# Kernel optimization log

Hardware: AMD Instinct MI355X
Metric: run time of the kernel (lower is better)

The kernel has to match this reference:

```python
import jax, jax.numpy as jnp
import numpy as np

LN_EPS = 1e-5   # torch LayerNorm default
NRM_EPS = 1e-8  # normalizer-state epsilon in mLSTMCell


def setup_inputs() -> dict:
    key = jax.random.key(0)
    ks = jax.random.split(key, 3)
    B, T, H, L, O = 32, 256, 1024, 4, 256
    x = jax.random.normal(ks[0], (B, T, H), dtype=jnp.float32)
    # 6 projections per layer in order (q, k, v, i, f, o); Linear stored as [in, out]
    W = jax.random.normal(ks[1], (L, 6, H, H), dtype=jnp.float32) * 0.02
    b = jnp.zeros((L, 6, H), dtype=jnp.float32)
    ln_g = jnp.ones((L, 6, H), dtype=jnp.float32)
    ln_b = jnp.zeros((L, 6, H), dtype=jnp.float32)
    fc_w = jax.random.normal(ks[2], (H, O), dtype=jnp.float32) * 0.02
    fc_b = jnp.zeros((O,), dtype=jnp.float32)
    return {"x": x, "W": W, "b": b, "ln_g": ln_g, "ln_b": ln_b,
            "fc_w": fc_w, "fc_b": fc_b}


def _layer_norm(z, g, beta):
    # z: [6, B, H]; g, beta: [6, H]
    mu = z.mean(-1, keepdims=True)
    var = z.var(-1, keepdims=True)
    return (z - mu) * jax.lax.rsqrt(var + LN_EPS) * g[:, None, :] + beta[:, None, :]


def _cell(x_in, h_prev, c_prev, n_prev, Wl, bl, gl, betal):
    # x_in: [B, H]; states: [B, H]; Wl: [6, H, H]
    z = jnp.einsum('bh,jhd->jbd', x_in, Wl) + bl[:, None, :]
    z = _layer_norm(z, gl, betal)
    q, k, v, zi, zf, zo = z  # q is computed by the original cell but unused
    i = jnp.exp(zi)
    f = jax.nn.sigmoid(zf)
    o = jax.nn.sigmoid(zo)
    # kv_interaction = outer(k, v); sum over dim=1 == sum(k) * v (same math, no [B,H,H])
    kv_sum = k.sum(-1, keepdims=True) * v
    c = f * c_prev + i * kv_sum
    n = f * n_prev + i * k
    n_hat = n / (jnp.linalg.norm(n, axis=-1, keepdims=True) + NRM_EPS)
    h = o * jnp.tanh(c * n_hat)
    return h, c, n


def _mlstm_forward(x, W, b, ln_g, ln_b, fc_w, fc_b):
    B, T, H = x.shape
    L = W.shape[0]
    h0 = jnp.zeros((L, B, H), x.dtype)
    init = (h0, h0, h0)  # (h, c, n)

    def step(carry, x_t):
        h, c, n = carry
        layer_in = x_t
        hs, cs, ns = [], [], []
        for l in range(L):  # small fixed layer count
            h_l, c_l, n_l = _cell(layer_in, h[l], c[l], n[l],
                                  W[l], b[l], ln_g[l], ln_b[l])
            if l > 0:  # residual connection (use_residual=True)
                h_l = h_l + layer_in
            layer_in = h_l
            hs.append(h_l); cs.append(c_l); ns.append(n_l)
        return (jnp.stack(hs), jnp.stack(cs), jnp.stack(ns)), None

    (h, c, n), _ = jax.lax.scan(step, init, jnp.swapaxes(x, 0, 1))
    # output[-1] == top-layer hidden at the final timestep
    out = h[-1] @ fc_w + fc_b  # [B, O]
    return out, (h, c, n)


def reference(x, W, b, ln_g, ln_b, fc_w, fc_b):
    return _mlstm_forward(x, W, b, ln_g, ln_b, fc_w, fc_b)
```

## Files before the change

### kernel.cpp

```cpp
#include <hip/hip_runtime.h>
#include <hip/hip_bf16.h>
#include <math.h>

#define H 1024
#define B 32
#define T 256
#define L 4
#define O 256
#define SEGLEN 16
#define NSEG (T / SEGLEN)

typedef _Float16 half8 __attribute__((ext_vector_type(8)));
typedef _Float16 half4 __attribute__((ext_vector_type(4)));
typedef float f32x4 __attribute__((ext_vector_type(4)));

#define X_PK_OFF   0
#define HB0_OFF    8388608
#define HB1_OFF    16777216
#define WT2_OFF    25165824
#define Z16_OFF    46137344
#define SEGA_OFF   88080384
#define SEGBC_OFF  89128960
#define SEGBN_OFF  90177536
#define STATS_OFF  91226112
#define CARC_OFF   91422720
#define CARN_OFF   92471296
#define FCP_OFF    93519872

__global__ __launch_bounds__(256) void pack_w(const float* __restrict__ W,
                                              _Float16* __restrict__ Wt2) {
  int tile = blockIdx.x;
  int m_idx = tile >> 8;
  int kt = (tile >> 4) & 15, ntt = tile & 15;
  int l = m_idx / 5, jj = m_idx % 5;
  const float* Wf = W + ((size_t)(l * 6 + jj + 1) << 20);
  _Float16* out = Wt2 + ((size_t)m_idx << 20);
  __shared__ float ts[64][65];
  int k0 = kt * 64, n0 = ntt * 64;
#pragma unroll
  for (int s = 0; s < 16; ++s) {
    int e = threadIdx.x + s * 256;
    int kk = e >> 6, col = e & 63;
    ts[kk][col] = Wf[(size_t)(k0 + kk) * H + n0 + col];
  }
  __syncthreads();
#pragma unroll
  for (int gi = 0; gi < 2; ++gi) {
    int g = threadIdx.x * 2 + gi;
    int l64 = g & 63, ksl = (g >> 6) & 1, ntl = g >> 7;
    int nn = l64 & 15, kh = l64 >> 4;
    half8 tmp;
#pragma unroll
    for (int e = 0; e < 8; ++e)
      tmp[e] = (_Float16)ts[ksl * 32 + kh * 8 + e][ntl * 16 + nn];
    *(half8*)&out[(size_t)((ntt * 4 + ntl) * 32 + kt * 2 + ksl) * 512 + (size_t)l64 * 8] = tmp;
  }
}

__global__ __launch_bounds__(256) void pack_x(const float* __restrict__ x,
                                              _Float16* __restrict__ x_pk) {
  int t = blockIdx.x;
  __shared__ float ld[32][257];
  for (int c = 0; c < 4; ++c) {
#pragma unroll
    for (int s = 0; s < 32; ++s) {
      int e2 = threadIdx.x + s * 256;
      int b = e2 >> 8, col = e2 & 255;
      ld[b][col] = x[((size_t)b * T + t) * H + c * 256 + col];
    }
    __syncthreads();
#pragma unroll
    for (int s3 = 0; s3 < 4; ++s3) {
      int gg = threadIdx.x * 4 + s3;
      int l64 = gg & 63, ksl = (gg >> 6) & 7, bt = gg >> 9;
      int nn = l64 & 15, kh = l64 >> 4;
      int b = bt * 16 + nn;
      half8 tmp;
#pragma unroll
      for (int e = 0; e < 8; ++e)
        tmp[e] = (_Float16)ld[b][ksl * 32 + kh * 8 + e];
      *(half8*)&x_pk[(size_t)t * 32768 + (size_t)bt * 16384 +
                     (size_t)(c * 8 + ksl) * 512 + (size_t)l64 * 8] = tmp;
    }
    __syncthreads();
  }
}

__global__ __launch_bounds__(512) void gemm_big(
    const _Float16* __restrict__ A_pk, const _Float16* __restrict__ Wl,
    _Float16* __restrict__ z16) {
  int raw = blockIdx.x;
  int xcd = raw & 7, c = raw >> 3;
  int bm = (xcd >> 1) * 16 + (c & 15);
  int bn = (xcd & 1) * 10 + (c >> 4);
  int w = threadIdx.x >> 6, lane = threadIdx.x & 63;
  int wm = w >> 2, wn = w & 3;

  __shared__ _Float16 smem[24576];

  int j = bn >> 2;
  const _Float16* gsrc[3];
  int ldst[3];
#pragma unroll
  for (int q = 0; q < 3; ++q) {
    int f = w * 3 + q;
    if (f < 8) {
      gsrc[q] = A_pk + (size_t)(bm * 8 + f) * 16384 + lane * 8;
      ldst[q] = f * 512 + lane * 8;
    } else {
      int nf = f - 8;
      gsrc[q] = Wl + ((size_t)j << 20) + (size_t)((bn & 3) * 16 + nf) * 16384 + lane * 8;
      ldst[q] = 4096 + nf * 512 + lane * 8;
    }
  }

  half8 stA[3], stB[3];
#pragma unroll
  for (int q = 0; q < 3; ++q) stA[q] = *(const half8*)(gsrc[q]);
#pragma unroll
  for (int q = 0; q < 3; ++q) *(half8*)&smem[ldst[q]] = stA[q];
#pragma unroll
  for (int q = 0; q < 3; ++q) stA[q] = *(const half8*)(gsrc[q] + 512);
  __syncthreads();

  f32x4 acc[4][4] = {};
  int ardo = wm * 2048 + lane * 8;
  int brdo = 4096 + wn * 2048 + lane * 8;

  for (int ks = 0; ks < 32; ks += 2) {
    {
      if (ks + 2 < 32) {
#pragma unroll
        for (int q = 0; q < 3; ++q)
          stB[q] = *(const half8*)(gsrc[q] + (size_t)(ks + 2) * 512);
      }
      half8 a[4], b[4];
#pragma unroll
      for (int i = 0; i < 4; ++i) a[i] = *(const half8*)&smem[ardo + i * 512];
#pragma unroll
      for (int i = 0; i < 4; ++i) b[i] = *(const half8*)&smem[brdo + i * 512];
#pragma unroll
      for (int i = 0; i < 4; ++i)
#pragma unroll
        for (int jf = 0; jf < 4; ++jf)
          acc[i][jf] = __builtin_amdgcn_mfma_f32_16x16x32_f16(a[i], b[jf], acc[i][jf], 0, 0, 0);
#pragma unroll
      for (int q = 0; q < 3; ++q) *(half8*)&smem[12288 + ldst[q]] = stA[q];
      asm volatile("s_waitcnt lgkmcnt(0)" ::: "memory");
      __builtin_amdgcn_s_barrier();
      __builtin_amdgcn_sched_barrier(0);
    }
    {
      if (ks + 3 < 32) {
#pragma unroll
        for (int q = 0; q < 3; ++q)
          stA[q] = *(const half8*)(gsrc[q] + (size_t)(ks + 3) * 512);
      }
      half8 a[4], b[4];
#pragma unroll
      for (int i = 0; i < 4; ++i) a[i] = *(const half8*)&smem[12288 + ardo + i * 512];
#pragma unroll
      for (int i = 0; i < 4; ++i) b[i] = *(const half8*)&smem[12288 + brdo + i * 512];
#pragma unroll
      for (int i = 0; i < 4; ++i)
#pragma unroll
        for (int jf = 0; jf < 4; ++jf)
          acc[i][jf] = __builtin_amdgcn_mfma_f32_16x16x32_f16(a[i], b[jf], acc[i][jf], 0, 0, 0);
      if (ks + 2 < 32) {
#pragma unroll
        for (int q = 0; q < 3; ++q) *(half8*)&smem[ldst[q]] = stB[q];
        asm volatile("s_waitcnt lgkmcnt(0)" ::: "memory");
        __builtin_amdgcn_s_barrier();
        __builtin_amdgcn_sched_barrier(0);
      }
    }
  }
  __syncthreads();

  _Float16 (*cz)[264] = (_Float16(*)[264])smem;
  int hb0 = (bn & 3) * 256;
  for (int p = 0; p < 2; ++p) {
    if (p) __syncthreads();
    if (wm == p) {
#pragma unroll
      for (int i = 0; i < 4; ++i)
#pragma unroll
        for (int jf = 0; jf < 4; ++jf)
#pragma unroll
          for (int r = 0; r < 4; ++r)
            cz[i * 16 + (lane >> 4) * 4 + r][wn * 64 + jf * 16 + (lane & 15)] =
                (_Float16)acc[i][jf][r];
    }
    __syncthreads();
#pragma unroll
    for (int s = 0; s < 4; ++s) {
      int e = threadIdx.x + s * 512;
      int r = e >> 5, h8 = e & 31;
      int m_local = bm * 128 + p * 64 + r;
      half8 vv = *(const half8*)&cz[r][h8 * 8];
      *(half8*)&z16[((size_t)m_local * 5 + j) * 1024 + hb0 + h8 * 8] = vv;
    }
  }
}

__global__ __launch_bounds__(256) void scan_p1fused(
    const _Float16* __restrict__ z16, const float* __restrict__ bias,
    const float* __restrict__ ln_g, const float* __restrict__ ln_b,
    float* __restrict__ stats, float* __restrict__ segA,
    float* __restrict__ segBc, float* __restrict__ segBn, int l) {
  int seg = blockIdx.x >> 5, b = blockIdx.x & 31;
  int tid = threadIdx.x, h0 = tid * 4;

  float bz[5][4], gg[5][4], bb[5][4];
#pragma unroll
  for (int jj = 0; jj < 5; ++jj) {
    float4 t1 = *(const float4*)&bias[(size_t)(l * 6 + 1 + jj) * H + h0];
    float4 t2 = *(const float4*)&ln_g[(size_t)(l * 6 + 1 + jj) * H + h0];
    float4 t3 = *(const float4*)&ln_b[(size_t)(l * 6 + 1 + jj) * H + h0];
    bz[jj][0] = t1.x; bz[jj][1] = t1.y; bz[jj][2] = t1.z; bz[jj][3] = t1.w;
    gg[jj][0] = t2.x; gg[jj][1] = t2.y; gg[jj][2] = t2.z; gg[jj][3] = t2.w;
    bb[jj][0] = t3.x; bb[jj][1] = t3.y; bb[jj][2] = t3.z; bb[jj][3] = t3.w;
  }

  float A[4] = {1.f, 1.f, 1.f, 1.f};
  float bc[4] = {0.f, 0.f, 0.f, 0.f};
  float bn[4] = {0.f, 0.f, 0.f, 0.f};
  __shared__ float sb[4][13];

  half4 zr[5];
  {
    int row0 = (seg * SEGLEN) * 32 + b;
#pragma unroll
    for (int jj = 0; jj < 5; ++jj)
      zr[jj] = *(const half4*)&z16[((size_t)row0 * 5 + jj) * 1024 + h0];
  }

  for (int u = 0; u < SEGLEN; ++u) {
    int row = (seg * SEGLEN + u) * 32 + b;
    half4 zc[5];
#pragma unroll
    for (int jj = 0; jj < 5; ++jj) zc[jj] = zr[jj];
    if (u + 1 < SEGLEN) {
      int rown = (seg * SEGLEN + u + 1) * 32 + b;
#pragma unroll
      for (int jj = 0; jj < 5; ++jj)
        zr[jj] = *(const half4*)&z16[((size_t)rown * 5 + jj) * 1024 + h0];
    }
    float v[5][4];
    float red[13];
#pragma unroll
    for (int jj = 0; jj < 5; ++jj) {
      float s = 0.f, sq = 0.f;
#pragma unroll
      for (int e = 0; e < 4; ++e) {
        float val = (float)zc[jj][e] + bz[jj][e];
        v[jj][e] = val;
        s += val;
        sq += val * val;
      }
      red[jj * 2] = s;
      red[jj * 2 + 1] = sq;
      if (jj == 0) {
        red[10] = v[0][0] * gg[0][0] + v[0][1] * gg[0][1] +
                  v[0][2] * gg[0][2] + v[0][3] * gg[0][3];
        red[11] = gg[0][0] + gg[0][1] + gg[0][2] + gg[0][3];
        red[12] = bb[0][0] + bb[0][1] + bb[0][2] + bb[0][3];
      }
    }
#pragma unroll
    for (int off = 32; off; off >>= 1)
#pragma unroll
      for (int q = 0; q < 13; ++q) red[q] += __shfl_xor(red[q], off);
    if ((tid & 63) == 0) {
#pragma unroll
      for (int q = 0; q < 13; ++q) sb[tid >> 6][q] = red[q];
    }
    __syncthreads();
    float st[13];
#pragma unroll
    for (int q = 0; q < 13; ++q)
      st[q] = sb[0][q] + sb[1][q] + sb[2][q] + sb[3][q];
    __syncthreads();

    float mus[5], rss[5];
#pragma unroll
    for (int jj = 0; jj < 5; ++jj) {
      float mu = st[jj * 2] * (1.0f / H);
      float var = st[jj * 2 + 1] * (1.0f / H) - mu * mu;
      mus[jj] = mu;
      rss[jj] = rsqrtf(var + 1e-5f);
    }
    float ksum = rss[0] * (st[10] - mus[0] * st[11]) + st[12];
    if (tid < 12) {
      float val;
      if (tid < 10) val = (tid & 1) ? rss[tid >> 1] : mus[tid >> 1];
      else if (tid == 10) val = ksum;
      else val = 0.f;
      stats[(size_t)row * 12 + tid] = val;
    }
#pragma unroll
    for (int e = 0; e < 4; ++e) {
      float k   = (v[0][e] - mus[0]) * rss[0] * gg[0][e] + bb[0][e];
      float vv  = (v[1][e] - mus[1]) * rss[1] * gg[1][e] + bb[1][e];
      float zi_ = (v[2][e] - mus[2]) * rss[2] * gg[2][e] + bb[2][e];
      float zf_ = (v[3][e] - mus[3]) * rss[3] * gg[3][e] + bb[3][e];
      float iv = __expf(zi_);
      float fv = 1.f / (1.f + __expf(-zf_));
      A[e] *= fv;
      bn[e] = fv * bn[e] + iv * k;
      bc[e] = fv * bc[e] + iv * (ksum * vv);
    }
  }
  size_t so = ((size_t)seg * 32 + b) * 1024 + h0;
  *(float4*)&segA[so]  = make_float4(A[0], A[1], A[2], A[3]);
  *(float4*)&segBn[so] = make_float4(bn[0], bn[1], bn[2], bn[3]);
  *(float4*)&segBc[so] = make_float4(bc[0], bc[1], bc[2], bc[3]);
}

__global__ __launch_bounds__(256) void scan_p2(
    const float* __restrict__ segA, const float* __restrict__ segBc,
    const float* __restrict__ segBn, float* __restrict__ carC,
    float* __restrict__ carN) {
  int idx = blockIdx.x * 256 + threadIdx.x;
  int h = idx & 1023, b = idx >> 10;
  float cc = 0.f, nn = 0.f;
#pragma unroll
  for (int seg = 0; seg < NSEG; ++seg) {
    size_t coff = (size_t)seg * 32768 + (size_t)b * 1024 + h;
    carC[coff] = cc;
    carN[coff] = nn;
    size_t so = ((size_t)seg * 32 + b) * 1024 + h;
    float a = segA[so];
    cc = segBc[so] + a * cc;
    nn = segBn[so] + a * nn;
  }
}

__global__ __launch_bounds__(256) void final_scan(
    const _Float16* __restrict__ z16, const float* __restrict__ stats,
    const float* __restrict__ bias, const float* __restrict__ ln_g,
    const float* __restrict__ ln_b, const float* __restrict__ carC,
    const float* __restrict__ carN, const _Float16* __restrict__ hin,
    _Float16* __restrict__ hout, float* __restrict__ out, int l) {
  int seg = blockIdx.x >> 5, b = blockIdx.x & 31;
  int tid = threadIdx.x, h0 = tid * 4;

  float bz[5][4], gg[5][4], bb[5][4];
#pragma unroll
  for (int jj = 0; jj < 5; ++jj) {
    float4 t1 = *(const float4*)&bias[(size_t)(l * 6 + 1 + jj) * H + h0];
    float4 t2 = *(const float4*)&ln_g[(size_t)(l * 6 + 1 + jj) * H + h0];
    float4 t3 = *(const float4*)&ln_b[(size_t)(l * 6 + 1 + jj) * H + h0];
    bz[jj][0] = t1.x; bz[jj][1] = t1.y; bz[jj][2] = t1.z; bz[jj][3] = t1.w;
    gg[jj][0] = t2.x; gg[jj][1] = t2.y; gg[jj][2] = t2.z; gg[jj][3] = t2.w;
    bb[jj][0] = t3.x; bb[jj][1] = t3.y; bb[jj][2] = t3.z; bb[jj][3] = t3.w;
  }

  size_t coff = (size_t)seg * 32768 + (size_t)b * 1024 + h0;
  float4 cC4 = *(const float4*)&carC[coff];
  float4 cN4 = *(const float4*)&carN[coff];
  float c_[4] = {cC4.x, cC4.y, cC4.z, cC4.w};
  float n_[4] = {cN4.x, cN4.y, cN4.z, cN4.w};

  size_t hfoff = (size_t)(b >> 4) * 16384 + (size_t)(h0 >> 5) * 512 +
                 (size_t)((((h0 & 31) >> 3) * 16) + (b & 15)) * 8 + (h0 & 7);
  __shared__ float sbuf[2][4];

  half4 zr[5];
  {
    int row0 = (seg * SEGLEN) * 32 + b;
#pragma unroll
    for (int jj = 0; jj < 5; ++jj)
      zr[jj] = *(const half4*)&z16[((size_t)row0 * 5 + jj) * 1024 + h0];
  }

  for (int u = 0; u < SEGLEN; ++u) {
    int t = seg * SEGLEN + u;
    int row = t * 32 + b;
    half4 zc[5];
#pragma unroll
    for (int jj = 0; jj < 5; ++jj) zc[jj] = zr[jj];
    if (u + 1 < SEGLEN) {
      int rown = (t + 1) * 32 + b;
#pragma unroll
      for (int jj = 0; jj < 5; ++jj)
        zr[jj] = *(const half4*)&z16[((size_t)rown * 5 + jj) * 1024 + h0];
    }
    half4 rin;
    if (l > 0) rin = *(const half4*)&hin[(size_t)t * 32768 + hfoff];

    const float* st = stats + (size_t)row * 12;
    float mu0 = st[0], rs0 = st[1], mu1 = st[2], rs1 = st[3];
    float mu2 = st[4], rs2 = st[5], mu3 = st[6], rs3 = st[7];
    float mu4 = st[8], rs4 = st[9], ksum = st[10];

    float ss = 0.f;
#pragma unroll
    for (int e = 0; e < 4; ++e) {
      float k   = ((float)zc[0][e] + bz[0][e] - mu0) * rs0 * gg[0][e] + bb[0][e];
      float v   = ((float)zc[1][e] + bz[1][e] - mu1) * rs1 * gg[1][e] + bb[1][e];
      float zi_ = ((float)zc[2][e] + bz[2][e] - mu2) * rs2 * gg[2][e] + bb[2][e];
      float zf_ = ((float)zc[3][e] + bz[3][e] - mu3) * rs3 * gg[3][e] + bb[3][e];
      float iv = __expf(zi_);
      float fv = 1.f / (1.f + __expf(-zf_));
      n_[e] = fv * n_[e] + iv * k;
      c_[e] = fv * c_[e] + iv * (ksum * v);
      ss += n_[e] * n_[e];
    }
#pragma unroll
    for (int off = 32; off; off >>= 1) ss += __shfl_down(ss, off);
    if ((tid & 63) == 0) sbuf[u & 1][tid >> 6] = ss;
    __syncthreads();
    float nrm = sbuf[u & 1][0] + sbuf[u & 1][1] + sbuf[u & 1][2] + sbuf[u & 1][3];
    float rn = 1.f / (sqrtf(nrm) + 1e-8f);

    float hh[4];
#pragma unroll
    for (int e = 0; e < 4; ++e) {
      float zo_ = ((float)zc[4][e] + bz[4][e] - mu4) * rs4 * gg[4][e] + bb[4][e];
      float ov = 1.f / (1.f + __expf(-zo_));
      float targ = c_[e] * (n_[e] * rn);
      float e2 = __expf(-2.f * fabsf(targ));
      float th = copysignf((1.f - e2) / (1.f + e2), targ);
      hh[e] = ov * th + ((l > 0) ? (float)rin[e] : 0.f);
    }
    half4 hx;
    hx[0] = (_Float16)hh[0]; hx[1] = (_Float16)hh[1];
    hx[2] = (_Float16)hh[2]; hx[3] = (_Float16)hh[3];
    *(half4*)&hout[(size_t)t * 32768 + hfoff] = hx;

    if (t == T - 1) {
      *(float4*)&out[8192 + (size_t)l * 32768 + (size_t)b * 1024 + h0] =
          make_float4(hh[0], hh[1], hh[2], hh[3]);
      *(float4*)&out[8192 + 131072 + ((size_t)(l * B) + b) * 1024 + h0] =
          make_float4(c_[0], c_[1], c_[2], c_[3]);
      *(float4*)&out[8192 + 262144 + ((size_t)(l * B) + b) * 1024 + h0] =
          make_float4(n_[0], n_[1], n_[2], n_[3]);
    }
  }
}

__global__ __launch_bounds__(256) void fc_part(
    const float* __restrict__ out_h, const float* __restrict__ fc_w,
    float* __restrict__ partial) {
  int b = blockIdx.x >> 3, kh = blockIdx.x & 7;
  int o = threadIdx.x;
  const float* hr = out_h + (size_t)b * 1024 + kh * 128;
  const float* wp = fc_w + (size_t)kh * 128 * O + o;
  float acc = 0.f;
#pragma unroll 8
  for (int h = 0; h < 128; ++h)
    acc = fmaf(hr[h], wp[(size_t)h * O], acc);
  partial[((size_t)kh * 32 + b) * O + o] = acc;
}

__global__ __launch_bounds__(256) void fc_reduce(
    const float* __restrict__ partial, const float* __restrict__ fc_b,
    float* __restrict__ out) {
  int b = blockIdx.x, o = threadIdx.x;
  float acc = fc_b[o];
#pragma unroll
  for (int kh = 0; kh < 8; ++kh)
    acc += partial[((size_t)kh * 32 + b) * O + o];
  out[(size_t)b * O + o] = acc;
}

extern "C" void kernel_launch(void* const* d_in, const int* in_sizes, int n_in,
                              void* d_out, int out_size, void* d_ws, size_t ws_size,
                              hipStream_t stream) {
  const float* x    = (const float*)d_in[0];
  const float* W    = (const float*)d_in[1];
  const float* bias = (const float*)d_in[2];
  const float* ln_g = (const float*)d_in[3];
  const float* ln_b = (const float*)d_in[4];
  const float* fc_w = (const float*)d_in[5];
  const float* fc_b = (const float*)d_in[6];
  float* out = (float*)d_out;
  _Float16* wsh = (_Float16*)d_ws;

  _Float16* x_pk = wsh + X_PK_OFF;
  _Float16* hb[2] = {wsh + HB0_OFF, wsh + HB1_OFF};
  _Float16* Wt2  = wsh + WT2_OFF;
  _Float16* z16  = wsh + Z16_OFF;
  float* segA  = (float*)(wsh + SEGA_OFF);
  float* segBc = (float*)(wsh + SEGBC_OFF);
  float* segBn = (float*)(wsh + SEGBN_OFF);
  float* stats = (float*)(wsh + STATS_OFF);
  float* carC  = (float*)(wsh + CARC_OFF);
  float* carN  = (float*)(wsh + CARN_OFF);
  float* fcp   = (float*)(wsh + FCP_OFF);

  pack_w<<<5120, 256, 0, stream>>>(W, Wt2);
  pack_x<<<256, 256, 0, stream>>>(x, x_pk);

  for (int l = 0; l < L; ++l) {
    const _Float16* A_in = (l == 0) ? x_pk : hb[(l - 1) & 1];
    _Float16* h_out = hb[l & 1];
    const _Float16* Wl = Wt2 + ((size_t)(l * 5) << 20);
    gemm_big<<<1280, 512, 0, stream>>>(A_in, Wl, z16);
    scan_p1fused<<<512, 256, 0, stream>>>(z16, bias, ln_g, ln_b, stats,
                                          segA, segBc, segBn, l);
    scan_p2<<<128, 256, 0, stream>>>(segA, segBc, segBn, carC, carN);
    final_scan<<<512, 256, 0, stream>>>(z16, stats, bias, ln_g, ln_b,
                                        carC, carN, A_in, h_out, out, l);
  }
  fc_part<<<256, 256, 0, stream>>>(out + 8192 + 3 * 32768, fc_w, fcp);
  fc_reduce<<<B, 256, 0, stream>>>(fcp, fc_b, out);
}
```

Before: 767.1 us.

## Halve scan segment length, merge pack kernels, slim per-step reductions

Scan segments shrink from 16 to 8 steps, doubling the block count of the segmented scan kernels to raise parallelism; workspace offsets are enlarged to match. The two packing kernels are merged into one launch to save a kernel launch. In the per-step layernorm reduction, the loop-invariant gamma/beta sums are hoisted out and reduced once. The shared reduction buffer is double-buffered so one __syncthreads per step can be dropped. A longer carry pass (scan_p2 over more segments) is the main added cost.

Result: slower. 784.2 us (+2.2%).

```diff
diff --git a/kernel.cpp b/kernel.cpp
--- a/kernel.cpp
+++ b/kernel.cpp
@@ -7,7 +7,7 @@
 #define T 256
 #define L 4
 #define O 256
-#define SEGLEN 16
+#define SEGLEN 8
 #define NSEG (T / SEGLEN)
 
 typedef _Float16 half8 __attribute__((ext_vector_type(8)));
@@ -20,69 +20,71 @@
 #define WT2_OFF    25165824
 #define Z16_OFF    46137344
 #define SEGA_OFF   88080384
-#define SEGBC_OFF  89128960
-#define SEGBN_OFF  90177536
-#define STATS_OFF  91226112
-#define CARC_OFF   91422720
-#define CARN_OFF   92471296
-#define FCP_OFF    93519872
-
-__global__ __launch_bounds__(256) void pack_w(const float* __restrict__ W,
-                                              _Float16* __restrict__ Wt2) {
-  int tile = blockIdx.x;
-  int m_idx = tile >> 8;
-  int kt = (tile >> 4) & 15, ntt = tile & 15;
-  int l = m_idx / 5, jj = m_idx % 5;
-  const float* Wf = W + ((size_t)(l * 6 + jj + 1) << 20);
-  _Float16* out = Wt2 + ((size_t)m_idx << 20);
-  __shared__ float ts[64][65];
-  int k0 = kt * 64, n0 = ntt * 64;
-#pragma unroll
-  for (int s = 0; s < 16; ++s) {
-    int e = threadIdx.x + s * 256;
-    int kk = e >> 6, col = e & 63;
-    ts[kk][col] = Wf[(size_t)(k0 + kk) * H + n0 + col];
-  }
-  __syncthreads();
-#pragma unroll
-  for (int gi = 0; gi < 2; ++gi) {
-    int g = threadIdx.x * 2 + gi;
-    int l64 = g & 63, ksl = (g >> 6) & 1, ntl = g >> 7;
-    int nn = l64 & 15, kh = l64 >> 4;
-    half8 tmp;
-#pragma unroll
-    for (int e = 0; e < 8; ++e)
-      tmp[e] = (_Float16)ts[ksl * 32 + kh * 8 + e][ntl * 16 + nn];
-    *(half8*)&out[(size_t)((ntt * 4 + ntl) * 32 + kt * 2 + ksl) * 512 + (size_t)l64 * 8] = tmp;
-  }
-}
-
-__global__ __launch_bounds__(256) void pack_x(const float* __restrict__ x,
-                                              _Float16* __restrict__ x_pk) {
-  int t = blockIdx.x;
-  __shared__ float ld[32][257];
-  for (int c = 0; c < 4; ++c) {
-#pragma unroll
-    for (int s = 0; s < 32; ++s) {
-      int e2 = threadIdx.x + s * 256;
-      int b = e2 >> 8, col = e2 & 255;
-      ld[b][col] = x[((size_t)b * T + t) * H + c * 256 + col];
+#define SEGBC_OFF  90177536
+#define SEGBN_OFF  92274688
+#define STATS_OFF  94371840
+#define CARC_OFF   94568448
+#define CARN_OFF   96665600
+#define FCP_OFF    98762752
+
+__global__ __launch_bounds__(256) void pack_wx(
+    const float* __restrict__ W, const float* __restrict__ x,
+    _Float16* __restrict__ Wt2, _Float16* __restrict__ x_pk) {
+  __shared__ float shmem[32 * 257];
+  if (blockIdx.x < 5120) {
+    int tile = blockIdx.x;
+    int m_idx = tile >> 8;
+    int kt = (tile >> 4) & 15, ntt = tile & 15;
+    int l = m_idx / 5, jj = m_idx % 5;
+    const float* Wf = W + ((size_t)(l * 6 + jj + 1) << 20);
+    _Float16* out = Wt2 + ((size_t)m_idx << 20);
+    float (*ts)[65] = (float(*)[65])shmem;
+    int k0 = kt * 64, n0 = ntt * 64;
+#pragma unroll
+    for (int s = 0; s < 16; ++s) {
+      int e = threadIdx.x + s * 256;
+      int kk = e >> 6, col = e & 63;
+      ts[kk][col] = Wf[(size_t)(k0 + kk) * H + n0 + col];
     }
     __syncthreads();
 #pragma unroll
-    for (int s3 = 0; s3 < 4; ++s3) {
-      int gg = threadIdx.x * 4 + s3;
-      int l64 = gg & 63, ksl = (gg >> 6) & 7, bt = gg >> 9;
+    for (int gi = 0; gi < 2; ++gi) {
+      int g = threadIdx.x * 2 + gi;
+      int l64 = g & 63, ksl = (g >> 6) & 1, ntl = g >> 7;
       int nn = l64 & 15, kh = l64 >> 4;
-      int b = bt * 16 + nn;
       half8 tmp;
 #pragma unroll
       for (int e = 0; e < 8; ++e)
-        tmp[e] = (_Float16)ld[b][ksl * 32 + kh * 8 + e];
-      *(half8*)&x_pk[(size_t)t * 32768 + (size_t)bt * 16384 +
-                     (size_t)(c * 8 + ksl) * 512 + (size_t)l64 * 8] = tmp;
-    }
-    __syncthreads();
+        tmp[e] = (_Float16)ts[ksl * 32 + kh * 8 + e][ntl * 16 + nn];
+      *(half8*)&out[(size_t)((ntt * 4 + ntl) * 32 + kt * 2 + ksl) * 512 +
+                    (size_t)l64 * 8] = tmp;
+    }
+  } else {
+    int t = blockIdx.x - 5120;
+    float (*ld)[257] = (float(*)[257])shmem;
+    for (int c = 0; c < 4; ++c) {
+      if (c) __syncthreads();
+#pragma unroll
+      for (int s = 0; s < 32; ++s) {
+        int e2 = threadIdx.x + s * 256;
+        int b = e2 >> 8, col = e2 & 255;
+        ld[b][col] = x[((size_t)b * T + t) * H + c * 256 + col];
+      }
+      __syncthreads();
+#pragma unroll
+      for (int s3 = 0; s3 < 4; ++s3) {
+        int gg = threadIdx.x * 4 + s3;
+        int l64 = gg & 63, ksl = (gg >> 6) & 7, bt = gg >> 9;
+        int nn = l64 & 15, kh = l64 >> 4;
+        int b = bt * 16 + nn;
+        half8 tmp;
+#pragma unroll
+        for (int e = 0; e < 8; ++e)
+          tmp[e] = (_Float16)ld[b][ksl * 32 + kh * 8 + e];
+        *(half8*)&x_pk[(size_t)t * 32768 + (size_t)bt * 16384 +
+                       (size_t)(c * 8 + ksl) * 512 + (size_t)l64 * 8] = tmp;
+      }
+    }
   }
 }
 
@@ -222,10 +224,25 @@
     bb[jj][0] = t3.x; bb[jj][1] = t3.y; bb[jj][2] = t3.z; bb[jj][3] = t3.w;
   }
 
+  __shared__ float sb[2][4][11];
+  __shared__ float sgb[8];
+  {
+    float r2[2] = {gg[0][0] + gg[0][1] + gg[0][2] + gg[0][3],
+                   bb[0][0] + bb[0][1] + bb[0][2] + bb[0][3]};
+#pragma unroll
+    for (int off = 32; off; off >>= 1) {
+      r2[0] += __shfl_xor(r2[0], off);
+      r2[1] += __shfl_xor(r2[1], off);
+    }
+    if ((tid & 63) == 0) { sgb[tid >> 6] = r2[0]; sgb[(tid >> 6) + 4] = r2[1]; }
+    __syncthreads();
+  }
+  float sgg = sgb[0] + sgb[1] + sgb[2] + sgb[3];
+  float sbb = sgb[4] + sgb[5] + sgb[6] + sgb[7];
+
   float A[4] = {1.f, 1.f, 1.f, 1.f};
   float bc[4] = {0.f, 0.f, 0.f, 0.f};
   float bn[4] = {0.f, 0.f, 0.f, 0.f};
-  __shared__ float sb[4][13];
 
   half4 zr[5];
   {
@@ -247,7 +264,7 @@
         zr[jj] = *(const half4*)&z16[((size_t)rown * 5 + jj) * 1024 + h0];
     }
     float v[5][4];
-    float red[13];
+    float red[11];
 #pragma unroll
     for (int jj = 0; jj < 5; ++jj) {
       float s = 0.f, sq = 0.f;
@@ -260,27 +277,22 @@
       }
       red[jj * 2] = s;
       red[jj * 2 + 1] = sq;
-      if (jj == 0) {
-        red[10] = v[0][0] * gg[0][0] + v[0][1] * gg[0][1] +
-                  v[0][2] * gg[0][2] + v[0][3] * gg[0][3];
-        red[11] = gg[0][0] + gg[0][1] + gg[0][2] + gg[0][3];
-        red[12] = bb[0][0] + bb[0][1] + bb[0][2] + bb[0][3];
-      }
-    }
+    }
+    red[10] = v[0][0] * gg[0][0] + v[0][1] * gg[0][1] +
+              v[0][2] * gg[0][2] + v[0][3] * gg[0][3];
 #pragma unroll
     for (int off = 32; off; off >>= 1)
 #pragma unroll
-      for (int q = 0; q < 13; ++q) red[q] += __shfl_xor(red[q], off);
+      for (int q = 0; q < 11; ++q) red[q] += __shfl_xor(red[q], off);
     if ((tid & 63) == 0) {
 #pragma unroll
-      for (int q = 0; q < 13; ++q) sb[tid >> 6][q] = red[q];
+      for (int q = 0; q < 11; ++q) sb[u & 1][tid >> 6][q] = red[q];
     }
     __syncthreads();
-    float st[13];
-#pragma unroll
-    for (int q = 0; q < 13; ++q)
-      st[q] = sb[0][q] + sb[1][q] + sb[2][q] + sb[3][q];
-    __syncthreads();
+    float st[11];
+#pragma unroll
+    for (int q = 0; q < 11; ++q)
+      st[q] = sb[u & 1][0][q] + sb[u & 1][1][q] + sb[u & 1][2][q] + sb[u & 1][3][q];
 
     float mus[5], rss[5];
 #pragma unroll
@@ -290,7 +302,7 @@
       mus[jj] = mu;
       rss[jj] = rsqrtf(var + 1e-5f);
     }
-    float ksum = rss[0] * (st[10] - mus[0] * st[11]) + st[12];
+    float ksum = rss[0] * (st[10] - mus[0] * sgg) + sbb;
     if (tid < 12) {
       float val;
       if (tid < 10) val = (tid & 1) ? rss[tid >> 1] : mus[tid >> 1];
@@ -490,19 +502,18 @@
   float* carN  = (float*)(wsh + CARN_OFF);
   float* fcp   = (float*)(wsh + FCP_OFF);
 
-  pack_w<<<5120, 256, 0, stream>>>(W, Wt2);
-  pack_x<<<256, 256, 0, stream>>>(x, x_pk);
+  pack_wx<<<5376, 256, 0, stream>>>(W, x, Wt2, x_pk);
 
   for (int l = 0; l < L; ++l) {
     const _Float16* A_in = (l == 0) ? x_pk : hb[(l - 1) & 1];
     _Float16* h_out = hb[l & 1];
     const _Float16* Wl = Wt2 + ((size_t)(l * 5) << 20);
     gemm_big<<<1280, 512, 0, stream>>>(A_in, Wl, z16);
-    scan_p1fused<<<512, 256, 0, stream>>>(z16, bias, ln_g, ln_b, stats,
-                                          segA, segBc, segBn, l);
+    scan_p1fused<<<NSEG * 32, 256, 0, stream>>>(z16, bias, ln_g, ln_b, stats,
+                                                segA, segBc, segBn, l);
     scan_p2<<<128, 256, 0, stream>>>(segA, segBc, segBn, carC, carN);
-    final_scan<<<512, 256, 0, stream>>>(z16, stats, bias, ln_g, ln_b,
-                                        carC, carN, A_in, h_out, out, l);
+    final_scan<<<NSEG * 32, 256, 0, stream>>>(z16, stats, bias, ln_g, ln_b,
+                                              carC, carN, A_in, h_out, out, l);
   }
   fc_part<<<256, 256, 0, stream>>>(out + 8192 + 3 * 32768, fc_w, fcp);
   fc_reduce<<<B, 256, 0, stream>>>(fcp, fc_b, out);
```
